# Performance work log

Hardware: AMD Instinct MI355X
Metric: run time of the kernel (lower is better)

## Reference

```python
import jax, jax.numpy as jnp
import numpy as np

BS, Z, NOBJ = 16384, 512, 64


def setup_inputs() -> dict:
    key = jax.random.key(0)
    ks = jax.random.split(key, 12)
    din = Z + 4  # z concatenated with bounds (x_size = 0)

    def lin(k, i, o):
        kw, kb = jax.random.split(k)
        w = jax.random.normal(kw, (i, o), jnp.float32) * (1.0 / np.sqrt(i))
        b = jax.random.normal(kb, (o,), jnp.float32) * 0.01
        return w, b

    W1, c1 = lin(ks[0], din, 512)
    W2, c2 = lin(ks[1], 512, 256)
    W3, c3 = lin(ks[2], 256, 128)
    W4, c4 = lin(ks[3], 128, 64)
    W5, c5 = lin(ks[4], 64, NOBJ * 4)
    z = jax.random.normal(ks[5], (BS, Z), jnp.float32)
    # room bounds [x_min, y_min, x_max, y_max]; must allow gaps >= 1
    bounds = jnp.array([0.0, 0.0, 40.0, 40.0], jnp.float32)
    return {"z": z, "bounds": bounds,
            "W1": W1, "c1": c1, "W2": W2, "c2": c2, "W3": W3, "c3": c3,
            "W4": W4, "c4": c4, "W5": W5, "c5": c5}


def _lrelu(v):
    return jnp.where(v > 0, v, 0.2 * v)


def _solve_axis(pp, pg, lo, hi):
    """Exact KKT solution of: min (x-pp)^2 + (g-pg)^2  s.t. x>=lo, g>=1, x+g<=hi.
    Returns (x, w) with w = x + g. Matches the parabolic QP per object/axis."""
    x0 = jnp.maximum(pp, lo)          # box projection (lower bounds only)
    g0 = jnp.maximum(pg, 1.0)
    t = 0.5 * (hi - pp - pg)          # projection of (pp,pg) onto line x+g=hi
    xl = jnp.clip(pp + t, lo, hi - 1.0)
    over = (x0 + g0) > hi             # coupling constraint active?
    x = jnp.where(over, xl, x0)
    g = jnp.where(over, hi - xl, g0)
    return x, x + g


def reference(z, bounds, W1, c1, W2, c2, W3, c3, W4, c4, W5, c5):
    bs = z.shape[0]
    bnd = jnp.broadcast_to(bounds, (bs, 4))
    h = jnp.concatenate([z, bnd], axis=1)          # (bs, z_size+4)
    h = _lrelu(h @ W1 + c1)                        # dropout treated as eval/identity
    h = _lrelu(h @ W2 + c2)
    h = _lrelu(h @ W3 + c3)
    h = _lrelu(h @ W4 + c4)
    p = (h @ W5 + c5).reshape(bs, NOBJ, 4)         # per-object params [px, py, pw, ph]
    px, py, pw, ph = p[..., 0], p[..., 1], p[..., 2], p[..., 3]
    b0, b1, b2, b3 = bounds[0], bounds[1], bounds[2], bounds[3]
    # QP objective: sum (x-px)^2+(y-py)^2+((w-x)-pw)^2+((h-y)-ph)^2
    # s.t. x>=b0, y>=b1, w<=b2, h<=b3, x<=w-1, y<=h-1. Separable per object/axis.
    xs, ws = _solve_axis(px, pw, b0, b2)
    ys, hs = _solve_axis(py, ph, b1, b3)
    return jnp.stack([xs, ys, ws, hs], axis=-1)    # (bs, num_objs, 4)
```

## Files before the change

### kernel.cpp

```cpp
#include <hip/hip_runtime.h>


#define MROWS 16384

typedef __attribute__((ext_vector_type(8))) short bf16x8;
typedef __attribute__((ext_vector_type(4))) float floatx4;

__device__ __forceinline__ unsigned short f2bf(float x) {
    union { float f; unsigned u; } c; c.f = x;
    unsigned r = c.u + 0x7fffu + ((c.u >> 16) & 1u);
    return (unsigned short)(r >> 16);
}
__device__ __forceinline__ float bf2f(unsigned short b) {
    union { unsigned u; float f; } c; c.u = ((unsigned)b) << 16;
    return c.f;
}

__device__ __forceinline__ bf16x8 gload(const unsigned short* p) {
    bf16x8 r;
    asm volatile("global_load_dwordx4 %0, %1, off"
                 : "=&v"(r)
                 : "v"((unsigned long long)(size_t)p)
                 : "memory");
    return r;
}
template<int IMM>
__device__ __forceinline__ void vwait(bf16x8& v) {
    asm volatile("s_waitcnt vmcnt(%1)" : "+v"(v) : "n"(IMM));
}
__device__ __forceinline__ void drain16(bf16x8 (&r)[16]) {
    asm volatile("s_waitcnt vmcnt(0)"
                 : "+v"(r[0]),  "+v"(r[1]),  "+v"(r[2]),  "+v"(r[3]),
                   "+v"(r[4]),  "+v"(r[5]),  "+v"(r[6]),  "+v"(r[7]),
                   "+v"(r[8]),  "+v"(r[9]),  "+v"(r[10]), "+v"(r[11]),
                   "+v"(r[12]), "+v"(r[13]), "+v"(r[14]), "+v"(r[15])
                 :: "memory");
}
__device__ __forceinline__ void drain8(bf16x8 (&r)[8]) {
    asm volatile("s_waitcnt vmcnt(0)"
                 : "+v"(r[0]), "+v"(r[1]), "+v"(r[2]), "+v"(r[3]),
                   "+v"(r[4]), "+v"(r[5]), "+v"(r[6]), "+v"(r[7])
                 :: "memory");
}
__device__ __forceinline__ void drain4(bf16x8 (&r)[4]) {
    asm volatile("s_waitcnt vmcnt(0)"
                 : "+v"(r[0]), "+v"(r[1]), "+v"(r[2]), "+v"(r[3])
                 :: "memory");
}

__global__ __launch_bounds__(256) void pack_wt(
    const float* __restrict__ W1, unsigned short* __restrict__ T1,
    const float* __restrict__ W2, unsigned short* __restrict__ T2,
    const float* __restrict__ W3, unsigned short* __restrict__ T3,
    const float* __restrict__ W4, unsigned short* __restrict__ T4,
    const float* __restrict__ W5, unsigned short* __restrict__ T5)
{
    const int idx = blockIdx.x * 256 + threadIdx.x;
    if (blockIdx.y == 4) {
        if (idx >= 2048) return;
        const int k8 = idx >> 8, n = idx & 255;
        const int ks = k8 >> 2, quad = k8 & 3;
        const int ntile = n >> 4, m_l = n & 15;
        unsigned short hi8[8], lo8[8];
        #pragma unroll
        for (int e = 0; e < 8; ++e) {
            const float v = W5[(k8 * 8 + e) * 256 + n];
            const unsigned short hi = f2bf(v);
            hi8[e] = hi; lo8[e] = f2bf(v - bf2f(hi));
        }
        const size_t b = (size_t)(((ks * 16 + ntile) * 2) * 64 + quad * 16 + m_l) * 8;
        *(uint4*)&T5[b]       = *(const uint4*)hi8;
        *(uint4*)&T5[b + 512] = *(const uint4*)lo8;
        return;
    }
    const float* W; unsigned short* T; int Kreal, nshift;
    switch (blockIdx.y) {
        case 0:  W = W1; T = T1; Kreal = 516; nshift = 9; break;
        case 1:  W = W2; T = T2; Kreal = 512; nshift = 8; break;
        case 2:  W = W3; T = T3; Kreal = 256; nshift = 7; break;
        default: W = W4; T = T4; Kreal = 128; nshift = 6; break;
    }
    const int N = 1 << nshift, NT = N >> 4;
    const int KS = (Kreal + 31) >> 5;
    if (idx >= N * KS * 4) return;
    const int k8 = idx >> nshift, n = idx & (N - 1);
    const int ks = k8 >> 2, quad = k8 & 3;
    const int ntile = n >> 4, m_l = n & 15;
    unsigned short t8[8];
    #pragma unroll
    for (int e = 0; e < 8; ++e) {
        const int k = k8 * 8 + e;
        t8[e] = (k < Kreal) ? f2bf(W[(size_t)k * N + n]) : (unsigned short)0;
    }
    *(uint4*)&T[(size_t)((ks * NT + ntile) * 64 + quad * 16 + m_l) * 8] = *(const uint4*)t8;
}

#define OFF_ZS   0
#define LD_ZS    552
#define OFF_H1   35328
#define LD_H1    520
#define OFF_H2   0
#define LD_H2    264
#define OFF_H3   16896
#define LD_H3    136
#define OFF_H4   25600
#define LD_H4    72
#define OFF_P    35328
#define LD_P     260
#define LDS_TOT  68608

template<int MR, int NF, int KSTEPS, int NT, int DEP>
__device__ __forceinline__ void layer_stream(
    unsigned short* lds, int offA, int lda, int offC, int ldc,
    const unsigned short* __restrict__ Wt,
    const float* __restrict__ bias, int ntile0, int rowbase, int lane)
{
    const int m_l = lane & 15, quad = lane >> 4;
    constexpr int NFR = NF * KSTEPS;
    static_assert(DEP <= NFR, "ring deeper than fragment stream");
    const unsigned short* __restrict__ Wb = Wt + ((size_t)ntile0 * 64 + lane) * 8;

    floatx4 acc[MR][NF];
    #pragma unroll
    for (int j = 0; j < NF; ++j) {
        const float bv = bias[ntile0 * 16 + j * 16 + m_l];
        #pragma unroll
        for (int m = 0; m < MR; ++m)
            acc[m][j] = (floatx4){bv, bv, bv, bv};
    }

    bf16x8 ring[DEP];
    #pragma unroll
    for (int f = 0; f < DEP; ++f) {
        const int g = (f < NFR) ? f : 0;
        ring[f] = gload(Wb + (size_t)((g / NF) * NT + (g % NF)) * 512);
    }
    bf16x8 a[MR], an[MR];
    #pragma unroll
    for (int m = 0; m < MR; ++m)
        a[m] = *(const bf16x8*)&lds[offA + (rowbase + m*16 + m_l) * lda + quad*8];
    #pragma unroll
    for (int f = 0; f < NFR; ++f) {
        const int ks = f / NF, j = f - ks * NF;
        if (j == 0 && ks + 1 < KSTEPS) {
            #pragma unroll
            for (int m = 0; m < MR; ++m)
                an[m] = *(const bf16x8*)&lds[offA + (rowbase + m*16 + m_l) * lda + (ks+1)*32 + quad*8];
        }
        vwait<DEP - 1>(ring[f % DEP]);
        #pragma unroll
        for (int m = 0; m < MR; ++m)
            acc[m][j] = __builtin_amdgcn_mfma_f32_16x16x32_bf16(a[m], ring[f % DEP], acc[m][j], 0, 0, 0);
        const int nf2 = (f + DEP < NFR) ? f + DEP : 0;
        ring[f % DEP] = gload(Wb + (size_t)((nf2 / NF) * NT + (nf2 % NF)) * 512);
        if (j == NF - 1 && ks + 1 < KSTEPS) {
            #pragma unroll
            for (int m = 0; m < MR; ++m) a[m] = an[m];
        }
    }
    if constexpr (DEP == 16) drain16(ring);
    else if constexpr (DEP == 8) drain8(ring);
    else drain4(ring);

    #pragma unroll
    for (int j = 0; j < NF; ++j) {
        const int col = ntile0 * 16 + j * 16 + m_l;
        #pragma unroll
        for (int m = 0; m < MR; ++m)
            #pragma unroll
            for (int r = 0; r < 4; ++r) {
                float v = acc[m][j][r];
                v = v > 0.f ? v : 0.2f * v;
                lds[offC + (rowbase + m*16 + quad*4 + r) * ldc + col] = f2bf(v);
            }
    }
}

__global__ __launch_bounds__(512, 2) void fused_mlp_qp(
    const float* __restrict__ z, const float* __restrict__ bounds,
    const unsigned short* __restrict__ Wt1, const float* __restrict__ c1,
    const unsigned short* __restrict__ Wt2, const float* __restrict__ c2,
    const unsigned short* __restrict__ Wt3, const float* __restrict__ c3,
    const unsigned short* __restrict__ Wt4, const float* __restrict__ c4,
    const unsigned short* __restrict__ Wt5, const float* __restrict__ c5,
    float* __restrict__ out)
{
    __shared__ unsigned short lds[LDS_TOT];
    const int tid  = threadIdx.x;
    const int wid  = tid >> 6, lane = tid & 63;
    const int m_l  = lane & 15, quad = lane >> 4;
    const int bm   = blockIdx.x * 64;

    const float4 bnd = *(const float4*)bounds;

    {
        const float4* __restrict__ zf = (const float4*)(z + (size_t)bm * 512);
        #pragma unroll
        for (int i = 0; i < 16; ++i) {
            const int f   = i * 512 + tid;
            const int row = f >> 7, c4i = f & 127;
            const float4 v = zf[f];
            unsigned short t4[4] = {f2bf(v.x), f2bf(v.y), f2bf(v.z), f2bf(v.w)};
            *(uint2*)&lds[OFF_ZS + row * LD_ZS + c4i * 4] = *(uint2*)t4;
        }
        if (tid < 320) {
            const int row = tid / 5, j = tid % 5;
            unsigned short t8[8] = {0,0,0,0,0,0,0,0};
            if (j == 0) { t8[0] = f2bf(bnd.x); t8[1] = f2bf(bnd.y);
                          t8[2] = f2bf(bnd.z); t8[3] = f2bf(bnd.w); }
            *(uint4*)&lds[OFF_ZS + row * LD_ZS + 512 + j * 8] = *(uint4*)t8;
        }
    }
    __syncthreads();

    layer_stream<4,4,17,32,16>(lds, OFF_ZS, LD_ZS, OFF_H1, LD_H1, Wt1, c1, wid*4, 0, lane);
    __syncthreads();
    layer_stream<4,2,16,16,16>(lds, OFF_H1, LD_H1, OFF_H2, LD_H2, Wt2, c2, wid*2, 0, lane);
    __syncthreads();
    layer_stream<4,1, 8, 8, 8>(lds, OFF_H2, LD_H2, OFF_H3, LD_H3, Wt3, c3, wid, 0, lane);
    __syncthreads();
    layer_stream<2,1, 4, 4, 4>(lds, OFF_H3, LD_H3, OFF_H4, LD_H4, Wt4, c4, wid & 3, (wid >> 2) * 32, lane);
    __syncthreads();

    {
        const unsigned short* __restrict__ Wb5 = Wt5 + (size_t)wid * 2048 + (size_t)lane * 8;
        floatx4 acc[4][2];
        #pragma unroll
        for (int j = 0; j < 2; ++j) {
            const float bv = c5[wid * 32 + j * 16 + m_l];
            #pragma unroll
            for (int m = 0; m < 4; ++m)
                acc[m][j] = (floatx4){bv, bv, bv, bv};
        }
        auto w5off = [](int g) {
            const int ks = g >> 2, rem = g & 3;
            return (size_t)ks * 16384 + (size_t)(rem >> 1) * 1024 + (size_t)(rem & 1) * 512;
        };
        bf16x8 ring[8];
        #pragma unroll
        for (int f = 0; f < 8; ++f) ring[f] = gload(Wb5 + w5off(f));
        bf16x8 a[2][4];
        #pragma unroll
        for (int ks = 0; ks < 2; ++ks)
            #pragma unroll
            for (int m = 0; m < 4; ++m)
                a[ks][m] = *(const bf16x8*)&lds[OFF_H4 + (m*16 + m_l) * LD_H4 + ks*32 + quad*8];
        #pragma unroll
        for (int f = 0; f < 8; ++f) {
            const int ks = f >> 2, rem = f & 3, j = rem >> 1;
            vwait<7>(ring[f]);
            #pragma unroll
            for (int m = 0; m < 4; ++m)
                acc[m][j] = __builtin_amdgcn_mfma_f32_16x16x32_bf16(a[ks][m], ring[f], acc[m][j], 0, 0, 0);
            ring[f] = gload(Wb5 + w5off(0));
        }
        drain8(ring);

        float* __restrict__ p = (float*)&lds[OFF_P];
        #pragma unroll
        for (int j = 0; j < 2; ++j) {
            const int col = wid * 32 + j * 16 + m_l;
            #pragma unroll
            for (int m = 0; m < 4; ++m)
                #pragma unroll
                for (int r = 0; r < 4; ++r)
                    p[(m*16 + quad*4 + r) * LD_P + col] = acc[m][j][r];
        }
    }
    __syncthreads();

    const float b0 = bnd.x, b1 = bnd.y, b2 = bnd.z, b3 = bnd.w;
    const float* __restrict__ p = (const float*)&lds[OFF_P];
    #pragma unroll
    for (int i = 0; i < 8; ++i) {
        const int row = i * 8 + wid;
        const float4 pv = *(const float4*)&p[row * LD_P + lane * 4];
        float xs, wo, ys, ho;
        {
            const float px = pv.x, pw = pv.z;
            const float x0 = fmaxf(px, b0);
            const float g0 = fmaxf(pw, 1.0f);
            const float t  = 0.5f * (b2 - px - pw);
            const float xl = fminf(fmaxf(px + t, b0), b2 - 1.0f);
            const bool over = (x0 + g0) > b2;
            const float x = over ? xl : x0;
            const float g = over ? (b2 - xl) : g0;
            xs = x; wo = x + g;
        }
        {
            const float py = pv.y, ph = pv.w;
            const float x0 = fmaxf(py, b1);
            const float g0 = fmaxf(ph, 1.0f);
            const float t  = 0.5f * (b3 - py - ph);
            const float xl = fminf(fmaxf(py + t, b1), b3 - 1.0f);
            const bool over = (x0 + g0) > b3;
            const float x = over ? xl : x0;
            const float g = over ? (b3 - xl) : g0;
            ys = x; ho = x + g;
        }
        float4 o; o.x = xs; o.y = ys; o.z = wo; o.w = ho;
        ((float4*)out)[(size_t)(bm + row) * 64 + lane] = o;
    }
}

extern "C" void kernel_launch(void* const* d_in, const int* in_sizes, int n_in,
                              void* d_out, int out_size, void* d_ws, size_t ws_size,
                              hipStream_t stream) {
    const float* z      = (const float*)d_in[0];
    const float* bounds = (const float*)d_in[1];
    const float* W1 = (const float*)d_in[2];
    const float* c1 = (const float*)d_in[3];
    const float* W2 = (const float*)d_in[4];
    const float* c2 = (const float*)d_in[5];
    const float* W3 = (const float*)d_in[6];
    const float* c3 = (const float*)d_in[7];
    const float* W4 = (const float*)d_in[8];
    const float* c4 = (const float*)d_in[9];
    const float* W5 = (const float*)d_in[10];
    const float* c5 = (const float*)d_in[11];
    float* out = (float*)d_out;

    unsigned short* ws  = (unsigned short*)d_ws;
    unsigned short* Wt1 = ws;
    unsigned short* Wt2 = Wt1 + 278528;
    unsigned short* Wt3 = Wt2 + 131072;
    unsigned short* Wt4 = Wt3 + 32768;
    unsigned short* Wt5 = Wt4 + 8192;

    pack_wt<<<dim3(136, 5), 256, 0, stream>>>(
        W1, Wt1, W2, Wt2, W3, Wt3, W4, Wt4, W5, Wt5);
    fused_mlp_qp<<<dim3(MROWS / 64), 512, 0, stream>>>(
        z, bounds, Wt1, c1, Wt2, c2, Wt3, c3, Wt4, c4, Wt5, c5, out);
}
```

Before: 119.4 us.

## Stream weight fragments continuously across layers with one shared prefetch ring

Replaces the per-layer weight prefetch ring, which was drained and refilled at every layer boundary, with one 16-deep ring that runs across all five layers. A global fragment index maps each slot to the right layer's packed weights, so loads for the next layer are already in flight during the current layer and its barrier. The first weight loads are issued before the z staging, biases are staged in LDS, and __syncthreads is replaced by an lgkmcnt-only wait plus s_barrier so outstanding global loads are not drained. The risk is that the barrier no longer waits on vector memory, and the more complex address computation may cost registers.

```diff
diff --git a/kernel.cpp b/kernel.cpp
--- a/kernel.cpp
+++ b/kernel.cpp
@@ -36,16 +36,8 @@
                    "+v"(r[12]), "+v"(r[13]), "+v"(r[14]), "+v"(r[15])
                  :: "memory");
 }
-__device__ __forceinline__ void drain8(bf16x8 (&r)[8]) {
-    asm volatile("s_waitcnt vmcnt(0)"
-                 : "+v"(r[0]), "+v"(r[1]), "+v"(r[2]), "+v"(r[3]),
-                   "+v"(r[4]), "+v"(r[5]), "+v"(r[6]), "+v"(r[7])
-                 :: "memory");
-}
-__device__ __forceinline__ void drain4(bf16x8 (&r)[4]) {
-    asm volatile("s_waitcnt vmcnt(0)"
-                 : "+v"(r[0]), "+v"(r[1]), "+v"(r[2]), "+v"(r[3])
-                 :: "memory");
+__device__ __forceinline__ void lds_barrier() {
+    asm volatile("s_waitcnt lgkmcnt(0)\n\ts_barrier" ::: "memory");
 }
 
 __global__ __launch_bounds__(256) void pack_wt(
@@ -107,19 +99,32 @@
 #define LD_H4    72
 #define OFF_P    35328
 #define LD_P     260
-#define LDS_TOT  68608
-
-template<int MR, int NF, int KSTEPS, int NT, int DEP>
-__device__ __forceinline__ void layer_stream(
-    unsigned short* lds, int offA, int lda, int offC, int ldc,
-    const unsigned short* __restrict__ Wt,
-    const float* __restrict__ bias, int ntile0, int rowbase, int lane)
+#define OFF_BF   68608
+#define LDS_TOT  71040
+
+struct WPlan {
+    const unsigned short* b0; const unsigned short* b1;
+    const unsigned short* b2; const unsigned short* b3;
+    const unsigned short* b4;
+};
+__device__ __forceinline__ const unsigned short* frag_addr(const WPlan& P, int g) {
+    if (g >= 120) g = 0;
+    if (g < 68)  { const int f = g;       return P.b0 + (size_t)((f >> 2) * 32 + (f & 3)) * 512; }
+    if (g < 100) { const int f = g - 68;  return P.b1 + (size_t)((f >> 1) * 16 + (f & 1)) * 512; }
+    if (g < 108) { const int f = g - 100; return P.b2 + (size_t)(f * 8) * 512; }
+    if (g < 112) { const int f = g - 108; return P.b3 + (size_t)(f * 4) * 512; }
+    { const int f = g - 112; const int ks = f >> 2, rem = f & 3;
+      return P.b4 + (size_t)ks * 16384 + (size_t)(rem >> 1) * 1024 + (size_t)(rem & 1) * 512; }
+}
+
+template<int MR, int NF, int KSTEPS, int G0>
+__device__ __forceinline__ void section(
+    bf16x8 (&ring)[16], unsigned short* lds, const WPlan& P,
+    int offA, int lda, int offC, int ldc,
+    const float* bias, int ntile0, int rowbase, int lane)
 {
     const int m_l = lane & 15, quad = lane >> 4;
     constexpr int NFR = NF * KSTEPS;
-    static_assert(DEP <= NFR, "ring deeper than fragment stream");
-    const unsigned short* __restrict__ Wb = Wt + ((size_t)ntile0 * 64 + lane) * 8;
-
     floatx4 acc[MR][NF];
     #pragma unroll
     for (int j = 0; j < NF; ++j) {
@@ -128,40 +133,28 @@
         for (int m = 0; m < MR; ++m)
             acc[m][j] = (floatx4){bv, bv, bv, bv};
     }
-
-    bf16x8 ring[DEP];
-    #pragma unroll
-    for (int f = 0; f < DEP; ++f) {
-        const int g = (f < NFR) ? f : 0;
-        ring[f] = gload(Wb + (size_t)((g / NF) * NT + (g % NF)) * 512);
-    }
     bf16x8 a[MR], an[MR];
     #pragma unroll
     for (int m = 0; m < MR; ++m)
         a[m] = *(const bf16x8*)&lds[offA + (rowbase + m*16 + m_l) * lda + quad*8];
     #pragma unroll
     for (int f = 0; f < NFR; ++f) {
-        const int ks = f / NF, j = f - ks * NF;
+        const int ks = f / NF, j = f - ks * NF, g = G0 + f;
         if (j == 0 && ks + 1 < KSTEPS) {
             #pragma unroll
             for (int m = 0; m < MR; ++m)
                 an[m] = *(const bf16x8*)&lds[offA + (rowbase + m*16 + m_l) * lda + (ks+1)*32 + quad*8];
         }
-        vwait<DEP - 1>(ring[f % DEP]);
+        vwait<15>(ring[g & 15]);
         #pragma unroll
         for (int m = 0; m < MR; ++m)
-            acc[m][j] = __builtin_amdgcn_mfma_f32_16x16x32_bf16(a[m], ring[f % DEP], acc[m][j], 0, 0, 0);
-        const int nf2 = (f + DEP < NFR) ? f + DEP : 0;
-        ring[f % DEP] = gload(Wb + (size_t)((nf2 / NF) * NT + (nf2 % NF)) * 512);
+            acc[m][j] = __builtin_amdgcn_mfma_f32_16x16x32_bf16(a[m], ring[g & 15], acc[m][j], 0, 0, 0);
+        ring[g & 15] = gload(frag_addr(P, g + 16));
         if (j == NF - 1 && ks + 1 < KSTEPS) {
             #pragma unroll
             for (int m = 0; m < MR; ++m) a[m] = an[m];
         }
     }
-    if constexpr (DEP == 16) drain16(ring);
-    else if constexpr (DEP == 8) drain8(ring);
-    else drain4(ring);
-
     #pragma unroll
     for (int j = 0; j < NF; ++j) {
         const int col = ntile0 * 16 + j * 16 + m_l;
@@ -193,6 +186,17 @@
 
     const float4 bnd = *(const float4*)bounds;
 
+    WPlan P;
+    P.b0 = Wt1 + ((size_t)(wid * 4) * 64 + lane) * 8;
+    P.b1 = Wt2 + ((size_t)(wid * 2) * 64 + lane) * 8;
+    P.b2 = Wt3 + ((size_t)wid * 64 + lane) * 8;
+    P.b3 = Wt4 + ((size_t)(wid & 3) * 64 + lane) * 8;
+    P.b4 = Wt5 + (size_t)wid * 2048 + (size_t)lane * 8;
+
+    bf16x8 ring[16];
+    #pragma unroll
+    for (int f = 0; f < 16; ++f) ring[f] = gload(frag_addr(P, f));
+
     {
         const float4* __restrict__ zf = (const float4*)(z + (size_t)bm * 512);
         #pragma unroll
@@ -210,35 +214,38 @@
                           t8[2] = f2bf(bnd.z); t8[3] = f2bf(bnd.w); }
             *(uint4*)&lds[OFF_ZS + row * LD_ZS + 512 + j * 8] = *(uint4*)t8;
         }
-    }
-    __syncthreads();
-
-    layer_stream<4,4,17,32,16>(lds, OFF_ZS, LD_ZS, OFF_H1, LD_H1, Wt1, c1, wid*4, 0, lane);
-    __syncthreads();
-    layer_stream<4,2,16,16,16>(lds, OFF_H1, LD_H1, OFF_H2, LD_H2, Wt2, c2, wid*2, 0, lane);
-    __syncthreads();
-    layer_stream<4,1, 8, 8, 8>(lds, OFF_H2, LD_H2, OFF_H3, LD_H3, Wt3, c3, wid, 0, lane);
-    __syncthreads();
-    layer_stream<2,1, 4, 4, 4>(lds, OFF_H3, LD_H3, OFF_H4, LD_H4, Wt4, c4, wid & 3, (wid >> 2) * 32, lane);
-    __syncthreads();
+        float* bf = (float*)&lds[OFF_BF];
+        for (int i = tid; i < 1216; i += 512) {
+            float v;
+            if      (i < 512)  v = c1[i];
+            else if (i < 768)  v = c2[i - 512];
+            else if (i < 896)  v = c3[i - 768];
+            else if (i < 960)  v = c4[i - 896];
+            else               v = c5[i - 960];
+            bf[i] = v;
+        }
+    }
+    lds_barrier();
+
+    const float* bf = (const float*)&lds[OFF_BF];
+    section<4,4,17,  0>(ring, lds, P, OFF_ZS, LD_ZS, OFF_H1, LD_H1, bf,       wid*4, 0, lane);
+    lds_barrier();
+    section<4,2,16, 68>(ring, lds, P, OFF_H1, LD_H1, OFF_H2, LD_H2, bf + 512, wid*2, 0, lane);
+    lds_barrier();
+    section<4,1, 8,100>(ring, lds, P, OFF_H2, LD_H2, OFF_H3, LD_H3, bf + 768, wid, 0, lane);
+    lds_barrier();
+    section<2,1, 4,108>(ring, lds, P, OFF_H3, LD_H3, OFF_H4, LD_H4, bf + 896, wid & 3, (wid >> 2) * 32, lane);
+    lds_barrier();
 
     {
-        const unsigned short* __restrict__ Wb5 = Wt5 + (size_t)wid * 2048 + (size_t)lane * 8;
         floatx4 acc[4][2];
         #pragma unroll
         for (int j = 0; j < 2; ++j) {
-            const float bv = c5[wid * 32 + j * 16 + m_l];
+            const float bv = bf[960 + wid * 32 + j * 16 + m_l];
             #pragma unroll
             for (int m = 0; m < 4; ++m)
                 acc[m][j] = (floatx4){bv, bv, bv, bv};
         }
-        auto w5off = [](int g) {
-            const int ks = g >> 2, rem = g & 3;
-            return (size_t)ks * 16384 + (size_t)(rem >> 1) * 1024 + (size_t)(rem & 1) * 512;
-        };
-        bf16x8 ring[8];
-        #pragma unroll
-        for (int f = 0; f < 8; ++f) ring[f] = gload(Wb5 + w5off(f));
         bf16x8 a[2][4];
         #pragma unroll
         for (int ks = 0; ks < 2; ++ks)
@@ -247,14 +254,14 @@
                 a[ks][m] = *(const bf16x8*)&lds[OFF_H4 + (m*16 + m_l) * LD_H4 + ks*32 + quad*8];
         #pragma unroll
         for (int f = 0; f < 8; ++f) {
-            const int ks = f >> 2, rem = f & 3, j = rem >> 1;
-            vwait<7>(ring[f]);
+            const int ks = f >> 2, rem = f & 3, j = rem >> 1, g = 112 + f;
+            vwait<15>(ring[g & 15]);
             #pragma unroll
             for (int m = 0; m < 4; ++m)
-                acc[m][j] = __builtin_amdgcn_mfma_f32_16x16x32_bf16(a[ks][m], ring[f], acc[m][j], 0, 0, 0);
-            ring[f] = gload(Wb5 + w5off(0));
-        }
-        drain8(ring);
+                acc[m][j] = __builtin_amdgcn_mfma_f32_16x16x32_bf16(a[ks][m], ring[g & 15], acc[m][j], 0, 0, 0);
+            ring[g & 15] = gload(frag_addr(P, g + 16));
+        }
+        drain16(ring);
 
         float* __restrict__ p = (float*)&lds[OFF_P];
         #pragma unroll
@@ -267,7 +274,7 @@
                     p[(m*16 + quad*4 + r) * LD_P + col] = acc[m][j][r];
         }
     }
-    __syncthreads();
+    lds_barrier();
 
     const float b0 = bnd.x, b1 = bnd.y, b2 = bnd.z, b3 = bnd.w;
     const float* __restrict__ p = (const float*)&lds[OFF_P];
```

Measured after the change: 115.6 us. 3.2% less time.
